# Performance work log

Hardware: AMD Instinct MI355X
Metric: run time of the kernel (lower is better)

Reference implementation:

```python
import jax, jax.numpy as jnp
import numpy as np

V = 32000; D = 1024; H = 16; L = 2; T = 2048; B = 4; C = 32000
DH = D // H
EPS = 1e-5


def layernorm(x, g, b):
    mu = jnp.mean(x, axis=-1, keepdims=True)
    var = jnp.mean((x - mu) ** 2, axis=-1, keepdims=True)
    return (x - mu) * jax.lax.rsqrt(var + EPS) * g + b


def setup_inputs() -> dict:
    key = jax.random.key(0)
    ks = jax.random.split(key, 16)
    s = 0.02
    return {
        "tokens": jax.random.randint(ks[0], (B, T), 0, V),
        "embed_W": jax.random.normal(ks[1], (V, D), jnp.float32) * s,
        "pos_W": jax.random.normal(ks[2], (T, D), jnp.float32) * s,
        "ln_g": jnp.ones((L, D), jnp.float32),
        "ln_b": jnp.zeros((L, D), jnp.float32),
        "qkv_W": jax.random.normal(ks[3], (L, D, 3 * D), jnp.float32) * s,
        "qkv_b": jnp.zeros((L, 3 * D), jnp.float32),
        "out_W": jax.random.normal(ks[4], (L, D, D), jnp.float32) * s,
        "out_b": jnp.zeros((L, D), jnp.float32),
        "lnf_g": jnp.ones((D,), jnp.float32),
        "lnf_b": jnp.zeros((D,), jnp.float32),
        "head_W": jax.random.normal(ks[5], (D, C), jnp.float32) * s,
        "head_b": jnp.zeros((C,), jnp.float32),
    }


def attn_block(x, g, b, Wqkv, bqkv, Wo, bo):
    # pre-LN attention + residual. NOTE: original module defines an MLP but never calls it.
    h = layernorm(x, g, b)
    qkv = h @ Wqkv + bqkv                      # [B,T,3D]
    q, k, v = jnp.split(qkv, 3, axis=-1)
    q = q.reshape(B, T, H, DH)
    k = k.reshape(B, T, H, DH)
    v = v.reshape(B, T, H, DH)
    scores = jnp.einsum("bqhd,bkhd->bhqk", q, k) / np.sqrt(DH)
    causal = jnp.tril(jnp.ones((T, T), bool))
    scores = jnp.where(causal, scores, -jnp.inf)
    attn = jax.nn.softmax(scores, axis=-1)
    o = jnp.einsum("bhqk,bkhd->bqhd", attn, v).reshape(B, T, D)
    return x + o @ Wo + bo


def reference(tokens, embed_W, pos_W, ln_g, ln_b, qkv_W, qkv_b, out_W, out_b,
              lnf_g, lnf_b, head_W, head_b):
    h = embed_W[tokens] + pos_W[jnp.arange(T)][None, :, :]   # [B,T,D]
    for i in range(L):
        h = attn_block(h, ln_g[i], ln_b[i], qkv_W[i], qkv_b[i], out_W[i], out_b[i])
    h = layernorm(h, lnf_g, lnf_b)
    logits = h[:, -1] @ head_W + head_b                      # [B,C]
    return logits
```

## Files before the change

kernel.cpp:

```cpp
#include <hip/hip_runtime.h>

typedef __attribute__((ext_vector_type(8))) __bf16 bf16x8;
typedef __attribute__((ext_vector_type(4))) __bf16 bf16x4;
typedef __attribute__((ext_vector_type(4))) float f32x4;

static constexpr int kB = 4, kT = 2048, kD = 1024, kH = 16, kDH = 64;
static constexpr int kC = 32000, kM = 8192, k3D = 3072;

#define MFMA16(a, b, c) __builtin_amdgcn_mfma_f32_16x16x32_bf16((a), (b), (c), 0, 0, 0)

__device__ __forceinline__ void gload_lds16(const __bf16* g, __bf16* l) {
  __builtin_amdgcn_global_load_lds(
      (const __attribute__((address_space(1))) unsigned int*)(const void*)g,
      (__attribute__((address_space(3))) unsigned int*)(void*)l, 16, 0, 0);
}

__global__ __launch_bounds__(256) void embed_kernel(const int* __restrict__ tok,
                                                    const float* __restrict__ embW,
                                                    const float* __restrict__ posW,
                                                    float* __restrict__ h) {
  const int row = blockIdx.x;
  const int t = row & (kT - 1);
  const int tk = tok[row];
  const f32x4 e = ((const f32x4*)(embW + (size_t)tk * kD))[threadIdx.x];
  const f32x4 p = ((const f32x4*)(posW + (size_t)t * kD))[threadIdx.x];
  ((f32x4*)(h + (size_t)row * kD))[threadIdx.x] = e + p;
}

template <bool BF16OUT>
__global__ __launch_bounds__(256) void ln_kernel(const float* __restrict__ x,
                                                 const float* __restrict__ g,
                                                 const float* __restrict__ bb,
                                                 void* __restrict__ outp) {
  const int row = blockIdx.x, tid = threadIdx.x;
  const f32x4 xv = ((const f32x4*)(x + (size_t)row * kD))[tid];
  float s  = xv[0] + xv[1] + xv[2] + xv[3];
  float s2 = xv[0]*xv[0] + xv[1]*xv[1] + xv[2]*xv[2] + xv[3]*xv[3];
  #pragma unroll
  for (int off = 1; off < 64; off <<= 1) {
    s  += __shfl_xor(s, off);
    s2 += __shfl_xor(s2, off);
  }
  __shared__ float red[8];
  const int w = tid >> 6;
  if ((tid & 63) == 0) { red[w*2] = s; red[w*2+1] = s2; }
  __syncthreads();
  s  = red[0] + red[2] + red[4] + red[6];
  s2 = red[1] + red[3] + red[5] + red[7];
  const float mu  = s * (1.f / kD);
  const float var = s2 * (1.f / kD) - mu * mu;
  const float rs  = rsqrtf(var + 1e-5f);
  const f32x4 gv = ((const f32x4*)g)[tid];
  const f32x4 bv = ((const f32x4*)bb)[tid];
  if constexpr (BF16OUT) {
    bf16x4 o;
    #pragma unroll
    for (int i = 0; i < 4; i++) o[i] = (__bf16)((xv[i] - mu) * rs * gv[i] + bv[i]);
    ((bf16x4*)((__bf16*)outp + (size_t)row * kD))[tid] = o;
  } else {
    f32x4 o;
    #pragma unroll
    for (int i = 0; i < 4; i++) o[i] = (xv[i] - mu) * rs * gv[i] + bv[i];
    ((f32x4*)((float*)outp + (size_t)row * kD))[tid] = o;
  }
}

__global__ __launch_bounds__(256) void transpose_w_kernel(const float* __restrict__ W,
                                                          __bf16* __restrict__ WT,
                                                          int K, int N) {
  __shared__ float sh[32][33];
  const int tx = threadIdx.x & 31, ty = threadIdx.x >> 5;
  const int ntile = N >> 5;
  const int c0 = (blockIdx.x % ntile) << 5;
  const int r0 = (blockIdx.x / ntile) << 5;
  #pragma unroll
  for (int i = 0; i < 4; i++) {
    const int r = ty + i * 8;
    sh[r][tx] = W[(size_t)(r0 + r) * N + c0 + tx];
  }
  __syncthreads();
  #pragma unroll
  for (int i = 0; i < 4; i++) {
    const int cc = ty + i * 8;
    WT[(size_t)(c0 + cc) * K + r0 + tx] = (__bf16)sh[tx][cc];
  }
}

template <bool OUT_BF16>
__global__ __launch_bounds__(256) void gemm_bt_kernel(const __bf16* __restrict__ A,
                                                      const __bf16* __restrict__ BT,
                                                      const float* __restrict__ bias,
                                                      const float* resid,
                                                      float* outf,
                                                      __bf16* outb,
                                                      int N, int K, int ldc,
                                                      int bm_mult, int bm_add) {
  __shared__ __bf16 As[128 * 64];
  __shared__ __bf16 Bs[128 * 64];
  const int tid = threadIdx.x;
  const int lane = tid & 63, w = tid >> 6;
  const int nbn = N >> 7;
  const int bm = (int)(blockIdx.x / nbn) * bm_mult + bm_add;
  const int bn = blockIdx.x % nbn;
  const int wr = (w >> 1) * 64, wc = (w & 1) * 64;
  const int lrow = lane & 15, lk8 = (lane >> 4) * 8;

  const int srow = lane >> 3;
  const int scol = (lane & 7) * 8;
  const __bf16* gA = A + (size_t)(bm * 128) * K;
  const __bf16* gB = BT + (size_t)(bn * 128) * K;

  f32x4 acc[4][4] = {};

  for (int k0 = 0; k0 < K; k0 += 64) {
    __syncthreads();
    #pragma unroll
    for (int i = 0; i < 4; i++) {
      const int c = w * 4 + i;
      const int row = c * 8 + srow;
      gload_lds16(gA + (size_t)row * K + k0 + scol, As + c * 512);
      gload_lds16(gB + (size_t)row * K + k0 + scol, Bs + c * 512);
    }
    __syncthreads();
    #pragma unroll
    for (int ks = 0; ks < 2; ks++) {
      bf16x8 af[4], bf[4];
      #pragma unroll
      for (int mt = 0; mt < 4; mt++)
        af[mt] = *(const bf16x8*)(As + (wr + mt * 16 + lrow) * 64 + ks * 32 + lk8);
      #pragma unroll
      for (int nt = 0; nt < 4; nt++)
        bf[nt] = *(const bf16x8*)(Bs + (wc + nt * 16 + lrow) * 64 + ks * 32 + lk8);
      #pragma unroll
      for (int mt = 0; mt < 4; mt++)
        #pragma unroll
        for (int nt = 0; nt < 4; nt++)
          acc[mt][nt] = MFMA16(af[mt], bf[nt], acc[mt][nt]);
    }
  }

  #pragma unroll
  for (int mt = 0; mt < 4; mt++) {
    const int row0 = bm * 128 + wr + mt * 16 + (lane >> 4) * 4;
    #pragma unroll
    for (int nt = 0; nt < 4; nt++) {
      const int col = bn * 128 + wc + nt * 16 + lrow;
      const float bsv = bias[col];
      #pragma unroll
      for (int r = 0; r < 4; r++) {
        const size_t idx = (size_t)(row0 + r) * ldc + col;
        const float v = acc[mt][nt][r] + bsv;
        if constexpr (OUT_BF16) {
          outb[idx] = (__bf16)v;
        } else {
          outf[idx] = v + resid[idx];
        }
      }
    }
  }
}

template <int MODE>
__global__ __launch_bounds__(256) void flash_kernel(const __bf16* __restrict__ qkv,
                                                    __bf16* __restrict__ o,
                                                    float* __restrict__ part_acc,
                                                    float* __restrict__ part_ml,
                                                    int nsub) {
  constexpr int LDK = 72;
  constexpr float SC = 0.18033688011112042f;
  __shared__ __bf16 Qs[64 * LDK];
  __shared__ __bf16 Ks[64 * LDK];
  __shared__ __bf16 Vt[64 * LDK];
  __shared__ __bf16 Ps[4][16 * LDK];
  const int tid = threadIdx.x, lane = tid & 63, w = tid >> 6;
  const int sub = (int)(blockIdx.x % nsub);
  const int bh = (int)(blockIdx.x / nsub);
  const int b = bh >> 4, hh = bh & 15;
  const int lrow = lane & 15, lk8 = (lane >> 4) * 8;
  const int NSUB = (MODE == 0) ? 2 : 1;

  for (int s = 0; s < NSUB; s++) {
    int qt, ktlo, kthi;
    if constexpr (MODE == 0) {
      qt = (s == 0) ? sub : (2 * nsub - 1 - sub);
      ktlo = 0; kthi = qt + 1;
    } else {
      qt = 31;
      ktlo = sub * (32 / 8); kthi = ktlo + 4;
    }

    #pragma unroll
    for (int q = 0; q < 2; q++) {
      const int c = tid + 256 * q;
      const int row = c >> 3, col = (c & 7) * 8;
      bf16x8 v = *(const bf16x8*)(qkv + (size_t)(b * kT + qt * 64 + row) * k3D + hh * kDH + col);
      *(bf16x8*)(Qs + row * LDK + col) = v;
    }
    __syncthreads();
    bf16x8 qf[2];
    qf[0] = *(const bf16x8*)(Qs + (w * 16 + lrow) * LDK + lk8);
    qf[1] = *(const bf16x8*)(Qs + (w * 16 + lrow) * LDK + 32 + lk8);

    float m_run[4] = {-1e30f, -1e30f, -1e30f, -1e30f};
    float l_run[4] = {0.f, 0.f, 0.f, 0.f};
    f32x4 acc[4] = {};

    for (int kt = ktlo; kt < kthi; kt++) {
      __syncthreads();
      #pragma unroll
      for (int q = 0; q < 2; q++) {
        const int c = tid + 256 * q;
        const int row = c >> 3, col = (c & 7) * 8;
        const size_t base = (size_t)(b * kT + kt * 64 + row) * k3D + hh * kDH + col;
        bf16x8 kv = *(const bf16x8*)(qkv + base + kD);
        *(bf16x8*)(Ks + row * LDK + col) = kv;
        bf16x8 vv = *(const bf16x8*)(qkv + base + 2 * kD);
        #pragma unroll
        for (int e = 0; e < 8; e++) {
          const int d = col + e;
          Vt[d * LDK + (row ^ (((d >> 3) & 7) << 3))] = vv[e];
        }
      }
      __syncthreads();

      f32x4 sv[4] = {};
      #pragma unroll
      for (int nt = 0; nt < 4; nt++) {
        #pragma unroll
        for (int ks = 0; ks < 2; ks++) {
          bf16x8 kf = *(const bf16x8*)(Ks + (nt * 16 + lrow) * LDK + ks * 32 + lk8);
          sv[nt] = MFMA16(qf[ks], kf, sv[nt]);
        }
      }
      #pragma unroll
      for (int nt = 0; nt < 4; nt++)
        #pragma unroll
        for (int r = 0; r < 4; r++) {
          float v = sv[nt][r] * SC;
          if (kt == qt) {
            const int colg = nt * 16 + lrow;
            const int rowg = w * 16 + (lane >> 4) * 4 + r;
            if (colg > rowg) v = -1e30f;
          }
          sv[nt][r] = v;
        }

      float f[4], psum[4];
      #pragma unroll
      for (int r = 0; r < 4; r++) {
        float mx = fmaxf(fmaxf(sv[0][r], sv[1][r]), fmaxf(sv[2][r], sv[3][r]));
        #pragma unroll
        for (int off = 1; off < 16; off <<= 1) mx = fmaxf(mx, __shfl_xor(mx, off));
        const float mnew = fmaxf(m_run[r], mx);
        f[r] = exp2f(m_run[r] - mnew);
        m_run[r] = mnew;
        psum[r] = 0.f;
      }
      #pragma unroll
      for (int nt = 0; nt < 4; nt++)
        #pragma unroll
        for (int r = 0; r < 4; r++) {
          const float p = exp2f(sv[nt][r] - m_run[r]);
          psum[r] += p;
          Ps[w][((lane >> 4) * 4 + r) * LDK + nt * 16 + lrow] = (__bf16)p;
        }
      #pragma unroll
      for (int r = 0; r < 4; r++) {
        float ps = psum[r];
        #pragma unroll
        for (int off = 1; off < 16; off <<= 1) ps += __shfl_xor(ps, off);
        l_run[r] = l_run[r] * f[r] + ps;
      }
      #pragma unroll
      for (int nt = 0; nt < 4; nt++)
        #pragma unroll
        for (int r = 0; r < 4; r++) acc[nt][r] *= f[r];

      asm volatile("s_waitcnt lgkmcnt(0)" ::: "memory");

      bf16x8 pf[2];
      pf[0] = *(const bf16x8*)(&Ps[w][lrow * LDK + lk8]);
      pf[1] = *(const bf16x8*)(&Ps[w][lrow * LDK + 32 + lk8]);
      #pragma unroll
      for (int nt = 0; nt < 4; nt++) {
        const int d = nt * 16 + lrow;
        const int swz = ((d >> 3) & 7) << 3;
        #pragma unroll
        for (int ks = 0; ks < 2; ks++) {
          bf16x8 vf = *(const bf16x8*)(Vt + d * LDK + ((ks * 32 + lk8) ^ swz));
          acc[nt] = MFMA16(pf[ks], vf, acc[nt]);
        }
      }
    }

    if constexpr (MODE == 0) {
      #pragma unroll
      for (int r = 0; r < 4; r++) {
        const int t = qt * 64 + w * 16 + (lane >> 4) * 4 + r;
        const float inv = 1.f / l_run[r];
        #pragma unroll
        for (int nt = 0; nt < 4; nt++)
          o[(size_t)(b * kT + t) * kD + hh * kDH + nt * 16 + lrow] = (__bf16)(acc[nt][r] * inv);
      }
    } else {
      const int tile = bh * nsub + sub;
      #pragma unroll
      for (int r = 0; r < 4; r++) {
        const int row = w * 16 + (lane >> 4) * 4 + r;
        #pragma unroll
        for (int nt = 0; nt < 4; nt++)
          part_acc[(size_t)tile * 4096 + row * 64 + nt * 16 + lrow] = acc[nt][r];
        if (lrow == 0) {
          part_ml[tile * 128 + row] = m_run[r];
          part_ml[tile * 128 + 64 + row] = l_run[r];
        }
      }
    }
  }
}

__global__ __launch_bounds__(256) void flash_merge_kernel(const float* __restrict__ part_acc,
                                                          const float* __restrict__ part_ml,
                                                          __bf16* __restrict__ o) {
  const int bh = blockIdx.x, b = bh >> 4, hh = bh & 15;
  for (int e = threadIdx.x; e < 4096; e += 256) {
    const int row = e >> 6, d = e & 63;
    float mstar = -1e30f;
    #pragma unroll
    for (int kc = 0; kc < 8; kc++)
      mstar = fmaxf(mstar, part_ml[(bh * 8 + kc) * 128 + row]);
    float lstar = 0.f, osum = 0.f;
    #pragma unroll
    for (int kc = 0; kc < 8; kc++) {
      const float wgt = exp2f(part_ml[(bh * 8 + kc) * 128 + row] - mstar);
      lstar += wgt * part_ml[(bh * 8 + kc) * 128 + 64 + row];
      osum  += wgt * part_acc[(size_t)(bh * 8 + kc) * 4096 + e];
    }
    o[(size_t)(b * kT + 1984 + row) * kD + hh * 64 + d] = (__bf16)(osum / lstar);
  }
}

__global__ __launch_bounds__(256) void proj_last_kernel(const __bf16* __restrict__ o,
                                                        const float* __restrict__ W,
                                                        const float* __restrict__ bias,
                                                        const float* __restrict__ h,
                                                        float* __restrict__ out4) {
  const int b = blockIdx.y;
  const int j = blockIdx.x * 256 + threadIdx.x;
  __shared__ float ov[kD];
  const __bf16* orow = o + (size_t)(b * kT + kT - 1) * kD;
  for (int i = threadIdx.x; i < kD; i += 256) ov[i] = (float)orow[i];
  __syncthreads();
  float acc = 0.f;
  #pragma unroll 8
  for (int k = 0; k < kD; k++) acc = fmaf(ov[k], W[(size_t)k * kD + j], acc);
  out4[b * kD + j] = h[(size_t)(b * kT + kT - 1) * kD + j] + bias[j] + acc;
}

__global__ __launch_bounds__(256) void head_kernel(const float* __restrict__ hl,
                                                   const float* __restrict__ W,
                                                   const float* __restrict__ hb,
                                                   float* __restrict__ out) {
  const int j = blockIdx.x * 256 + threadIdx.x;
  __shared__ float sh[kB * kD];
  for (int i = threadIdx.x; i < kB * kD; i += 256) sh[i] = hl[i];
  __syncthreads();
  float a0 = 0.f, a1 = 0.f, a2 = 0.f, a3 = 0.f;
  #pragma unroll 8
  for (int k = 0; k < kD; k++) {
    const float wv = W[(size_t)k * kC + j];
    a0 = fmaf(sh[k], wv, a0);
    a1 = fmaf(sh[kD + k], wv, a1);
    a2 = fmaf(sh[2 * kD + k], wv, a2);
    a3 = fmaf(sh[3 * kD + k], wv, a3);
  }
  const float bb = hb[j];
  out[j] = a0 + bb;
  out[kC + j] = a1 + bb;
  out[2 * kC + j] = a2 + bb;
  out[3 * kC + j] = a3 + bb;
}

extern "C" void kernel_launch(void* const* d_in, const int* in_sizes, int n_in,
                              void* d_out, int out_size, void* d_ws, size_t ws_size,
                              hipStream_t stream) {
  const int*   tokens = (const int*)d_in[0];
  const float* embW   = (const float*)d_in[1];
  const float* posW   = (const float*)d_in[2];
  const float* ln_g   = (const float*)d_in[3];
  const float* ln_b   = (const float*)d_in[4];
  const float* qkv_W  = (const float*)d_in[5];
  const float* qkv_b  = (const float*)d_in[6];
  const float* out_W  = (const float*)d_in[7];
  const float* out_b  = (const float*)d_in[8];
  const float* lnf_g  = (const float*)d_in[9];
  const float* lnf_b  = (const float*)d_in[10];
  const float* headW  = (const float*)d_in[11];
  const float* headb  = (const float*)d_in[12];
  float* logits = (float*)d_out;

  char* ws = (char*)d_ws;
  float*  h     = (float*)(ws);
  __bf16* hn    = (__bf16*)(ws + 33554432);
  __bf16* qkv   = (__bf16*)(ws + 50331648);
  __bf16* ob    = (__bf16*)(ws + 100663296);
  __bf16* WqkvT = (__bf16*)(ws + 117440512);
  __bf16* WoT   = (__bf16*)(ws + 130023424);
  float*  hl4   = (float*)(ws + 132120576);
  float*  hl    = (float*)(ws + 132136960);
  float* part_acc = (float*)(ws + 33554432);
  float* part_ml  = (float*)(ws + 33554432 + 8388608);

  transpose_w_kernel<<<(kD/32)*(k3D/32), 256, 0, stream>>>(qkv_W, WqkvT, kD, k3D);
  transpose_w_kernel<<<(kD/32)*(k3D/32), 256, 0, stream>>>(qkv_W + (size_t)kD*k3D,
                                                           WqkvT + (size_t)k3D*kD, kD, k3D);
  transpose_w_kernel<<<(kD/32)*(kD/32), 256, 0, stream>>>(out_W, WoT, kD, kD);

  embed_kernel<<<kM, 256, 0, stream>>>(tokens, embW, posW, h);

  ln_kernel<true><<<kM, 256, 0, stream>>>(h, ln_g, ln_b, hn);
  gemm_bt_kernel<true><<<(kM/128)*(k3D/128), 256, 0, stream>>>(
      hn, WqkvT, qkv_b, nullptr, nullptr, qkv, k3D, kD, k3D, 1, 0);
  flash_kernel<0><<<kB*kH*16, 256, 0, stream>>>(qkv, ob, nullptr, nullptr, 16);
  gemm_bt_kernel<false><<<(kM/128)*(kD/128), 256, 0, stream>>>(
      ob, WoT, out_b, h, h, nullptr, kD, kD, kD, 1, 0);

  ln_kernel<true><<<kM, 256, 0, stream>>>(h, ln_g + kD, ln_b + kD, hn);
  gemm_bt_kernel<true><<<(kM/128)*(2048/128), 256, 0, stream>>>(
      hn, WqkvT + (size_t)k3D*kD + (size_t)kD*kD, qkv_b + k3D + kD,
      nullptr, nullptr, qkv + kD, 2048, kD, k3D, 1, 0);
  gemm_bt_kernel<true><<<kB*(kD/128), 256, 0, stream>>>(
      hn, WqkvT + (size_t)k3D*kD, qkv_b + k3D,
      nullptr, nullptr, qkv, kD, kD, k3D, 16, 15);
  flash_kernel<1><<<kB*kH*8, 256, 0, stream>>>(qkv, nullptr, part_acc, part_ml, 8);
  flash_merge_kernel<<<kB*kH, 256, 0, stream>>>(part_acc, part_ml, ob);
  proj_last_kernel<<<dim3(kD/256, kB), 256, 0, stream>>>(ob, out_W + (size_t)kD*kD,
                                                         out_b + kD, h, hl4);

  ln_kernel<false><<<kB, 256, 0, stream>>>(hl4, lnf_g, lnf_b, hl);
  head_kernel<<<kC/256, 256, 0, stream>>>(hl, headW, headb, logits);
}
```

Measured before the change: 570.8 us.

## Emit pre-transposed V from QKV GEMM and restructure flash attention with direct LDS loads

The QKV GEMM epilogue now writes V directly into a per-head transposed [b,h,d,t] buffer, and Q/K are stored in a narrower 2048-column buffer. Flash attention loads Q, K and V^T via global_load_lds with XOR swizzle, pre-scales Q, and computes S^T so each lane owns one query row. This removes the scalar V transpose in LDS and the P round-trip through shared memory, replacing the latter with lane shuffles. Both kernels also remap workgroup IDs across XCDs. The cost is extra strided epilogue stores in the GEMM and more shuffle traffic.

```diff
diff --git a/kernel.cpp b/kernel.cpp
--- a/kernel.cpp
+++ b/kernel.cpp
@@ -3,9 +3,10 @@
 typedef __attribute__((ext_vector_type(8))) __bf16 bf16x8;
 typedef __attribute__((ext_vector_type(4))) __bf16 bf16x4;
 typedef __attribute__((ext_vector_type(4))) float f32x4;
-
-static constexpr int kB = 4, kT = 2048, kD = 1024, kH = 16, kDH = 64;
-static constexpr int kC = 32000, kM = 8192, k3D = 3072;
+typedef unsigned long long ull;
+
+static constexpr int kB = 4, kT = 2048, kD = 1024, kH = 16;
+static constexpr int kC = 32000, kM = 8192, k3D = 3072, kQK = 2048;
 
 #define MFMA16(a, b, c) __builtin_amdgcn_mfma_f32_16x16x32_bf16((a), (b), (c), 0, 0, 0)
 
@@ -93,15 +94,19 @@
                                                       const float* resid,
                                                       float* outf,
                                                       __bf16* outb,
-                                                      int N, int K, int ldc,
+                                                      __bf16* vtp,
+                                                      int N, int K, int ldc, int vt_c0,
                                                       int bm_mult, int bm_add) {
   __shared__ __bf16 As[128 * 64];
   __shared__ __bf16 Bs[128 * 64];
   const int tid = threadIdx.x;
   const int lane = tid & 63, w = tid >> 6;
+  int wg = (int)blockIdx.x;
+  const int nwg = gridDim.x;
+  wg = (wg & 7) * (nwg >> 3) + (wg >> 3);
   const int nbn = N >> 7;
-  const int bm = (int)(blockIdx.x / nbn) * bm_mult + bm_add;
-  const int bn = blockIdx.x % nbn;
+  const int bm = (wg / nbn) * bm_mult + bm_add;
+  const int bn = wg % nbn;
   const int wr = (w >> 1) * 64, wc = (w & 1) * 64;
   const int lrow = lane & 15, lk8 = (lane >> 4) * 8;
 
@@ -146,14 +151,23 @@
     for (int nt = 0; nt < 4; nt++) {
       const int col = bn * 128 + wc + nt * 16 + lrow;
       const float bsv = bias[col];
-      #pragma unroll
-      for (int r = 0; r < 4; r++) {
-        const size_t idx = (size_t)(row0 + r) * ldc + col;
-        const float v = acc[mt][nt][r] + bsv;
-        if constexpr (OUT_BF16) {
-          outb[idx] = (__bf16)v;
-        } else {
-          outf[idx] = v + resid[idx];
+      if (vtp && col >= vt_c0) {
+        const int vd = col - vt_c0;
+        const int bb_ = row0 >> 11, t = row0 & (kT - 1);
+        bf16x4 pk;
+        #pragma unroll
+        for (int r = 0; r < 4; r++) pk[r] = (__bf16)(acc[mt][nt][r] + bsv);
+        *(bf16x4*)(vtp + ((size_t)((bb_ << 4) + (vd >> 6)) * 64 + (vd & 63)) * kT + t) = pk;
+      } else {
+        #pragma unroll
+        for (int r = 0; r < 4; r++) {
+          const size_t idx = (size_t)(row0 + r) * ldc + col;
+          const float v = acc[mt][nt][r] + bsv;
+          if constexpr (OUT_BF16) {
+            outb[idx] = (__bf16)v;
+          } else {
+            outf[idx] = v + resid[idx];
+          }
         }
       }
     }
@@ -162,158 +176,170 @@
 
 template <int MODE>
 __global__ __launch_bounds__(256) void flash_kernel(const __bf16* __restrict__ qkv,
+                                                    const __bf16* __restrict__ vtg,
                                                     __bf16* __restrict__ o,
                                                     float* __restrict__ part_acc,
                                                     float* __restrict__ part_ml,
                                                     int nsub) {
-  constexpr int LDK = 72;
   constexpr float SC = 0.18033688011112042f;
-  __shared__ __bf16 Qs[64 * LDK];
-  __shared__ __bf16 Ks[64 * LDK];
-  __shared__ __bf16 Vt[64 * LDK];
-  __shared__ __bf16 Ps[4][16 * LDK];
+  __shared__ __bf16 Qs[64 * 64];
+  __shared__ __bf16 Ks[64 * 64];
+  __shared__ __bf16 Vs[64 * 64];
   const int tid = threadIdx.x, lane = tid & 63, w = tid >> 6;
-  const int sub = (int)(blockIdx.x % nsub);
-  const int bh = (int)(blockIdx.x / nsub);
+  int wg = (int)blockIdx.x;
+  const int nwg = gridDim.x;
+  wg = (wg & 7) * (nwg >> 3) + (wg >> 3);
+  const int sub = wg % nsub, bh = wg / nsub;
   const int b = bh >> 4, hh = bh & 15;
-  const int lrow = lane & 15, lk8 = (lane >> 4) * 8;
-  const int NSUB = (MODE == 0) ? 2 : 1;
-
-  for (int s = 0; s < NSUB; s++) {
+  const int g = lane >> 4, qown = lane & 15;
+  const int sslot = (lane & 7) ^ ((lane >> 3) & 7);
+  const int swz = (qown & 7) << 3;
+  const size_t row0 = (size_t)b * kT;
+  const int NS = (MODE == 0) ? 2 : 1;
+
+  for (int s = 0; s < NS; s++) {
     int qt, ktlo, kthi;
     if constexpr (MODE == 0) {
-      qt = (s == 0) ? sub : (2 * nsub - 1 - sub);
+      qt = s ? (2 * nsub - 1 - sub) : sub;
       ktlo = 0; kthi = qt + 1;
     } else {
-      qt = 31;
-      ktlo = sub * (32 / 8); kthi = ktlo + 4;
-    }
-
-    #pragma unroll
-    for (int q = 0; q < 2; q++) {
-      const int c = tid + 256 * q;
-      const int row = c >> 3, col = (c & 7) * 8;
-      bf16x8 v = *(const bf16x8*)(qkv + (size_t)(b * kT + qt * 64 + row) * k3D + hh * kDH + col);
-      *(bf16x8*)(Qs + row * LDK + col) = v;
+      qt = 31; ktlo = sub * 4; kthi = ktlo + 4;
+    }
+
+    __syncthreads();
+    #pragma unroll
+    for (int j = 0; j < 2; j++) {
+      const int r = w * 16 + j * 8 + (lane >> 3);
+      gload_lds16(qkv + (row0 + qt * 64 + r) * kQK + hh * 64 + sslot * 8,
+                  Qs + (w * 16 + j * 8) * 64);
     }
     __syncthreads();
     bf16x8 qf[2];
-    qf[0] = *(const bf16x8*)(Qs + (w * 16 + lrow) * LDK + lk8);
-    qf[1] = *(const bf16x8*)(Qs + (w * 16 + lrow) * LDK + 32 + lk8);
-
-    float m_run[4] = {-1e30f, -1e30f, -1e30f, -1e30f};
-    float l_run[4] = {0.f, 0.f, 0.f, 0.f};
+    #pragma unroll
+    for (int ks = 0; ks < 2; ks++) {
+      bf16x8 qr = *(const bf16x8*)(Qs + (w * 16 + qown) * 64 + ((ks * 32 + 8 * g) ^ swz));
+      #pragma unroll
+      for (int i = 0; i < 8; i++) qf[ks][i] = (__bf16)((float)qr[i] * SC);
+    }
+
+    float m_run = -1e30f, l_run = 0.f;
     f32x4 acc[4] = {};
 
     for (int kt = ktlo; kt < kthi; kt++) {
       __syncthreads();
       #pragma unroll
-      for (int q = 0; q < 2; q++) {
-        const int c = tid + 256 * q;
-        const int row = c >> 3, col = (c & 7) * 8;
-        const size_t base = (size_t)(b * kT + kt * 64 + row) * k3D + hh * kDH + col;
-        bf16x8 kv = *(const bf16x8*)(qkv + base + kD);
-        *(bf16x8*)(Ks + row * LDK + col) = kv;
-        bf16x8 vv = *(const bf16x8*)(qkv + base + 2 * kD);
-        #pragma unroll
-        for (int e = 0; e < 8; e++) {
-          const int d = col + e;
-          Vt[d * LDK + (row ^ (((d >> 3) & 7) << 3))] = vv[e];
+      for (int j = 0; j < 2; j++) {
+        const int r = w * 16 + j * 8 + (lane >> 3);
+        gload_lds16(qkv + (row0 + kt * 64 + r) * kQK + 1024 + hh * 64 + sslot * 8,
+                    Ks + (w * 16 + j * 8) * 64);
+        gload_lds16(vtg + ((size_t)bh * 64 + r) * kT + kt * 64 + sslot * 8,
+                    Vs + (w * 16 + j * 8) * 64);
+      }
+      __syncthreads();
+
+      f32x4 sv[4] = {};
+      #pragma unroll
+      for (int nt = 0; nt < 4; nt++) {
+        const int kr = nt * 16 + qown;
+        #pragma unroll
+        for (int ks = 0; ks < 2; ks++) {
+          bf16x8 kf = *(const bf16x8*)(Ks + kr * 64 + ((ks * 32 + 8 * g) ^ swz));
+          sv[nt] = MFMA16(kf, qf[ks], sv[nt]);
         }
       }
-      __syncthreads();
-
-      f32x4 sv[4] = {};
+      if (kt == qt) {
+        #pragma unroll
+        for (int nt = 0; nt < 4; nt++)
+          #pragma unroll
+          for (int r = 0; r < 4; r++)
+            if (nt * 16 + 4 * g + r > w * 16 + qown) sv[nt][r] = -1e30f;
+      }
+
+      float mx = -1e30f;
+      #pragma unroll
+      for (int nt = 0; nt < 4; nt++)
+        #pragma unroll
+        for (int r = 0; r < 4; r++) mx = fmaxf(mx, sv[nt][r]);
+      mx = fmaxf(mx, __shfl_xor(mx, 16));
+      mx = fmaxf(mx, __shfl_xor(mx, 32));
+      const float mnew = fmaxf(m_run, mx);
+      const float fsc = exp2f(m_run - mnew);
+      m_run = mnew;
+      float ps = 0.f;
+      ull quad[4];
       #pragma unroll
       for (int nt = 0; nt < 4; nt++) {
+        union { bf16x4 v; ull u; } qd;
+        #pragma unroll
+        for (int r = 0; r < 4; r++) {
+          const float p = exp2f(sv[nt][r] - mnew);
+          ps += p;
+          qd.v[r] = (__bf16)p;
+        }
+        quad[nt] = qd.u;
+      }
+      ps += __shfl_xor(ps, 16);
+      ps += __shfl_xor(ps, 32);
+      l_run = l_run * fsc + ps;
+
+      float fr[4];
+      #pragma unroll
+      for (int r = 0; r < 4; r++) fr[r] = __shfl(fsc, 20 * g + r);
+      #pragma unroll
+      for (int nt = 0; nt < 4; nt++)
+        #pragma unroll
+        for (int r = 0; r < 4; r++) acc[nt][r] *= fr[r];
+
+      bf16x8 pf[2];
+      #pragma unroll
+      for (int ks = 0; ks < 2; ks++) {
+        const int src = (g & 1) * 32 + qown;
+        const ull t0 = __shfl(quad[2 * ks],     src);
+        const ull t1 = __shfl(quad[2 * ks + 1], src);
+        const ull lo = (g & 2) ? t1 : t0;
+        const ull t2 = __shfl(quad[2 * ks],     src + 16);
+        const ull t3 = __shfl(quad[2 * ks + 1], src + 16);
+        const ull hi = (g & 2) ? t3 : t2;
+        union { ull u[2]; bf16x8 v; } pk;
+        pk.u[0] = lo; pk.u[1] = hi;
+        pf[ks] = pk.v;
+      }
+
+      #pragma unroll
+      for (int nt = 0; nt < 4; nt++) {
+        const int vr = nt * 16 + qown;
         #pragma unroll
         for (int ks = 0; ks < 2; ks++) {
-          bf16x8 kf = *(const bf16x8*)(Ks + (nt * 16 + lrow) * LDK + ks * 32 + lk8);
-          sv[nt] = MFMA16(qf[ks], kf, sv[nt]);
-        }
-      }
-      #pragma unroll
-      for (int nt = 0; nt < 4; nt++)
-        #pragma unroll
-        for (int r = 0; r < 4; r++) {
-          float v = sv[nt][r] * SC;
-          if (kt == qt) {
-            const int colg = nt * 16 + lrow;
-            const int rowg = w * 16 + (lane >> 4) * 4 + r;
-            if (colg > rowg) v = -1e30f;
-          }
-          sv[nt][r] = v;
-        }
-
-      float f[4], psum[4];
-      #pragma unroll
-      for (int r = 0; r < 4; r++) {
-        float mx = fmaxf(fmaxf(sv[0][r], sv[1][r]), fmaxf(sv[2][r], sv[3][r]));
-        #pragma unroll
-        for (int off = 1; off < 16; off <<= 1) mx = fmaxf(mx, __shfl_xor(mx, off));
-        const float mnew = fmaxf(m_run[r], mx);
-        f[r] = exp2f(m_run[r] - mnew);
-        m_run[r] = mnew;
-        psum[r] = 0.f;
-      }
-      #pragma unroll
-      for (int nt = 0; nt < 4; nt++)
-        #pragma unroll
-        for (int r = 0; r < 4; r++) {
-          const float p = exp2f(sv[nt][r] - m_run[r]);
-          psum[r] += p;
-          Ps[w][((lane >> 4) * 4 + r) * LDK + nt * 16 + lrow] = (__bf16)p;
-        }
-      #pragma unroll
-      for (int r = 0; r < 4; r++) {
-        float ps = psum[r];
-        #pragma unroll
-        for (int off = 1; off < 16; off <<= 1) ps += __shfl_xor(ps, off);
-        l_run[r] = l_run[r] * f[r] + ps;
-      }
-      #pragma unroll
-      for (int nt = 0; nt < 4; nt++)
-        #pragma unroll
-        for (int r = 0; r < 4; r++) acc[nt][r] *= f[r];
-
-      asm volatile("s_waitcnt lgkmcnt(0)" ::: "memory");
-
-      bf16x8 pf[2];
-      pf[0] = *(const bf16x8*)(&Ps[w][lrow * LDK + lk8]);
-      pf[1] = *(const bf16x8*)(&Ps[w][lrow * LDK + 32 + lk8]);
-      #pragma unroll
-      for (int nt = 0; nt < 4; nt++) {
-        const int d = nt * 16 + lrow;
-        const int swz = ((d >> 3) & 7) << 3;
-        #pragma unroll
-        for (int ks = 0; ks < 2; ks++) {
-          bf16x8 vf = *(const bf16x8*)(Vt + d * LDK + ((ks * 32 + lk8) ^ swz));
+          bf16x8 vf = *(const bf16x8*)(Vs + vr * 64 + ((ks * 32 + 8 * g) ^ swz));
           acc[nt] = MFMA16(pf[ks], vf, acc[nt]);
         }
       }
     }
 
     if constexpr (MODE == 0) {
+      const float li = 1.f / l_run;
+      float lr[4];
+      #pragma unroll
+      for (int r = 0; r < 4; r++) lr[r] = __shfl(li, 20 * g + r);
       #pragma unroll
       for (int r = 0; r < 4; r++) {
-        const int t = qt * 64 + w * 16 + (lane >> 4) * 4 + r;
-        const float inv = 1.f / l_run[r];
+        const int t = qt * 64 + w * 16 + 4 * g + r;
         #pragma unroll
         for (int nt = 0; nt < 4; nt++)
-          o[(size_t)(b * kT + t) * kD + hh * kDH + nt * 16 + lrow] = (__bf16)(acc[nt][r] * inv);
+          o[(row0 + t) * kD + hh * 64 + nt * 16 + qown] = (__bf16)(acc[nt][r] * lr[r]);
       }
     } else {
       const int tile = bh * nsub + sub;
       #pragma unroll
       for (int r = 0; r < 4; r++) {
-        const int row = w * 16 + (lane >> 4) * 4 + r;
+        const int rr = w * 16 + 4 * g + r;
         #pragma unroll
         for (int nt = 0; nt < 4; nt++)
-          part_acc[(size_t)tile * 4096 + row * 64 + nt * 16 + lrow] = acc[nt][r];
-        if (lrow == 0) {
-          part_ml[tile * 128 + row] = m_run[r];
-          part_ml[tile * 128 + 64 + row] = l_run[r];
-        }
+          part_acc[(size_t)tile * 4096 + rr * 64 + nt * 16 + qown] = acc[nt][r];
+      }
+      if (g == 0) {
+        part_ml[tile * 128 + w * 16 + qown] = m_run;
+        part_ml[tile * 128 + 64 + w * 16 + qown] = l_run;
       }
     }
   }
@@ -403,11 +429,12 @@
   float*  h     = (float*)(ws);
   __bf16* hn    = (__bf16*)(ws + 33554432);
   __bf16* qkv   = (__bf16*)(ws + 50331648);
+  __bf16* Vt    = (__bf16*)(ws + 83886080);
   __bf16* ob    = (__bf16*)(ws + 100663296);
   __bf16* WqkvT = (__bf16*)(ws + 117440512);
-  __bf16* WoT   = (__bf16*)(ws + 130023424);
-  float*  hl4   = (float*)(ws + 132120576);
-  float*  hl    = (float*)(ws + 132136960);
+  __bf16* WoT   = (__bf16*)(ws + 130613248);
+  float*  hl4   = (float*)(ws + 132710400);
+  float*  hl    = (float*)(ws + 132726784);
   float* part_acc = (float*)(ws + 33554432);
   float* part_ml  = (float*)(ws + 33554432 + 8388608);
 
@@ -420,19 +447,19 @@
 
   ln_kernel<true><<<kM, 256, 0, stream>>>(h, ln_g, ln_b, hn);
   gemm_bt_kernel<true><<<(kM/128)*(k3D/128), 256, 0, stream>>>(
-      hn, WqkvT, qkv_b, nullptr, nullptr, qkv, k3D, kD, k3D, 1, 0);
-  flash_kernel<0><<<kB*kH*16, 256, 0, stream>>>(qkv, ob, nullptr, nullptr, 16);
+      hn, WqkvT, qkv_b, nullptr, nullptr, qkv, Vt, k3D, kD, kQK, 2048, 1, 0);
+  flash_kernel<0><<<kB*kH*16, 256, 0, stream>>>(qkv, Vt, ob, nullptr, nullptr, 16);
   gemm_bt_kernel<false><<<(kM/128)*(kD/128), 256, 0, stream>>>(
-      ob, WoT, out_b, h, h, nullptr, kD, kD, kD, 1, 0);
+      ob, WoT, out_b, h, h, nullptr, nullptr, kD, kD, kD, 1 << 30, 1, 0);
 
   ln_kernel<true><<<kM, 256, 0, stream>>>(h, ln_g + kD, ln_b + kD, hn);
   gemm_bt_kernel<true><<<(kM/128)*(2048/128), 256, 0, stream>>>(
       hn, WqkvT + (size_t)k3D*kD + (size_t)kD*kD, qkv_b + k3D + kD,
-      nullptr, nullptr, qkv + kD, 2048, kD, k3D, 1, 0);
+      nullptr, nullptr, qkv + 1024, Vt, 2048, kD, kQK, 1024, 1, 0);
   gemm_bt_kernel<true><<<kB*(kD/128), 256, 0, stream>>>(
       hn, WqkvT + (size_t)k3D*kD, qkv_b + k3D,
-      nullptr, nullptr, qkv, kD, kD, k3D, 16, 15);
-  flash_kernel<1><<<kB*kH*8, 256, 0, stream>>>(qkv, nullptr, part_acc, part_ml, 8);
+      nullptr, nullptr, qkv, nullptr, kD, kD, kQK, 1 << 30, 16, 15);
+  flash_kernel<1><<<kB*kH*8, 256, 0, stream>>>(qkv, Vt, nullptr, part_acc, part_ml, 8);
   flash_merge_kernel<<<kB*kH, 256, 0, stream>>>(part_acc, part_ml, ob);
   proj_last_kernel<<<dim3(kD/256, kB), 256, 0, stream>>>(ob, out_W + (size_t)kD*kD,
                                                          out_b + kD, h, hl4);
```

Measured after the change: 535.1 us. 1.07x faster.
